# Optimization experiments

Measured on AMD Instinct MI355X. Metric: run time of the kernel, lower is better.

## Reference

```python
import jax, jax.numpy as jnp
import numpy as np

N, D, T, ET, E = 100000, 128, 3, 4, 250000


def gru_cell(m, h, w_ih, w_hh, b_ih, b_hh):
    # torch.nn.GRUCell semantics
    gi = m @ w_ih.T + b_ih          # [N, 3D]
    gh = h @ w_hh.T + b_hh          # [N, 3D]
    i_r, i_z, i_n = jnp.split(gi, 3, axis=1)
    h_r, h_z, h_n = jnp.split(gh, 3, axis=1)
    r = jax.nn.sigmoid(i_r + h_r)
    z = jax.nn.sigmoid(i_z + h_z)
    n = jnp.tanh(i_n + r * h_n)
    return (1.0 - z) * n + z * h


def setup_inputs() -> dict:
    key = jax.random.key(0)
    ks = jax.random.split(key, 10)
    x = jax.random.normal(ks[0], (N, D), dtype=jnp.float32)
    edge_row = jax.random.randint(ks[1], (ET, E), 0, N, dtype=jnp.int32)
    edge_col = jax.random.randint(ks[2], (ET, E), 0, N, dtype=jnp.int32)
    edge_val = jnp.ones((ET, E), dtype=jnp.float32)
    xav = float(np.sqrt(6.0 / (D + D)))  # xavier_uniform per (D,D) slice
    weight = jax.random.uniform(ks[3], (T, ET, D, D), jnp.float32, -xav, xav)
    bias_w = jax.random.uniform(ks[4], (T, ET, D), jnp.float32, -0.01, 0.01)
    s = float(1.0 / np.sqrt(D))  # GRUCell default init range
    w_ih = jax.random.uniform(ks[5], (3 * D, D), jnp.float32, -s, s)
    w_hh = jax.random.uniform(ks[6], (3 * D, D), jnp.float32, -s, s)
    b_ih = jax.random.uniform(ks[7], (3 * D,), jnp.float32, -s, s)
    b_hh = jax.random.uniform(ks[8], (3 * D,), jnp.float32, -s, s)
    return {"x": x, "edge_row": edge_row, "edge_col": edge_col,
            "edge_val": edge_val, "weight": weight, "bias_w": bias_w,
            "w_ih": w_ih, "w_hh": w_hh, "b_ih": b_ih, "b_hh": b_hh}


def reference(x, edge_row, edge_col, edge_val, weight, bias_w, w_ih, w_hh, b_ih, b_hh):
    n_nodes = x.shape[0]
    h = x  # input_dim == out_channels, no zero-padding needed
    num_t = weight.shape[0]

    def agg_one(m_e, col_e, row_e, val_e):
        # sparse.mm: out[row] += val * m[col]
        msg = m_e[col_e] * val_e[:, None]                 # [E, D]
        return jax.ops.segment_sum(msg, row_e, num_segments=n_nodes)

    for t in range(num_t):
        # per-edge-type dense transform: [ET, N, D]
        m = jnp.einsum('nd,edf->enf', h, weight[t]) + bias_w[t][:, None, :]
        agg = jax.vmap(agg_one)(m, edge_col, edge_row, edge_val)  # [ET, N, D]
        m_sum = agg.sum(axis=0)                                    # [N, D]
        h = gru_cell(m_sum, h, w_ih, w_hh, b_ih, b_hh)
    return h
```

## Files before the change

### kernel.cpp

```cpp
#include <hip/hip_runtime.h>
#include <stdint.h>

#define NN  100000
#define DD  128
#define TT  3
#define ETT 4
#define EE  250000
#define NCH 49
#define GRUGRID 512

typedef float  f32x4  __attribute__((ext_vector_type(4)));
typedef __bf16 bf16x8 __attribute__((ext_vector_type(8)));

__device__ __forceinline__ float bf2f(uint32_t u){ u <<= 16; return __builtin_bit_cast(float, u); }
__device__ __forceinline__ uint32_t f2bf(float f){
  uint32_t u = __builtin_bit_cast(uint32_t, f);
  return (u + 0x7FFFu + ((u >> 16) & 1u)) >> 16;
}
__device__ __forceinline__ f32x4 mfma16(bf16x8 a, bf16x8 b, f32x4 c){
  return __builtin_amdgcn_mfma_f32_16x16x32_bf16(a, b, c, 0, 0, 0);
}

__global__ void k_count(const int* __restrict__ erow, const float* __restrict__ eval,
                        int* __restrict__ counts, float* __restrict__ degval){
  int idx = blockIdx.x * 256 + threadIdx.x;
  if (idx >= ETT * EE) return;
  int e = idx / EE;
  int row = erow[idx];
  atomicAdd(&counts[e * NN + row], 1);
  atomicAdd(&degval[e * NN + row], eval[idx]);
}

__global__ void k_blksum(const int* __restrict__ counts, int* __restrict__ bsum){
  const int b = blockIdx.x, e = b / NCH, c = b % NCH;
  const int* p = counts + e * NN + c * 2048;
  int lim = NN - c * 2048; if (lim > 2048) lim = 2048;
  const int t = threadIdx.x;
  int s = 0;
  #pragma unroll
  for (int i = 0; i < 8; ++i){
    int idx = i * 256 + t;
    if (idx < lim) s += p[idx];
  }
  #pragma unroll
  for (int d = 32; d; d >>= 1) s += __shfl_down(s, d);
  __shared__ int wsum[4];
  if ((t & 63) == 0) wsum[t >> 6] = s;
  __syncthreads();
  if (t == 0) bsum[b] = wsum[0] + wsum[1] + wsum[2] + wsum[3];
}

__global__ void k_scanp(const int* __restrict__ bsum, int* __restrict__ bexc,
                        int* __restrict__ offsets){
  const int t = threadIdx.x, wid = t >> 6, l = t & 63;
  int v = (l < NCH) ? bsum[wid * NCH + l] : 0;
  int x = v;
  #pragma unroll
  for (int d = 1; d < 64; d <<= 1){ int y = __shfl_up(x, d); if (l >= d) x += y; }
  if (l < NCH) bexc[wid * NCH + l] = x - v;
  if (l == NCH - 1) offsets[wid * (NN + 1) + NN] = x;
}

__global__ void k_apply(const int* __restrict__ counts, const int* __restrict__ bexc,
                        int* __restrict__ offsets){
  const int b = blockIdx.x, e = b / NCH, c = b % NCH;
  const int* p = counts + e * NN + c * 2048;
  int* off = offsets + e * (NN + 1) + c * 2048;
  int lim = NN - c * 2048; if (lim > 2048) lim = 2048;
  const int t = threadIdx.x, l = t & 63, wid = t >> 6;
  __shared__ int wt[4];
  int v[8], s = 0;
  #pragma unroll
  for (int i = 0; i < 8; ++i){
    int idx = t * 8 + i;
    v[i] = (idx < lim) ? p[idx] : 0; s += v[i];
  }
  int x = s;
  #pragma unroll
  for (int d = 1; d < 64; d <<= 1){ int y = __shfl_up(x, d); if (l >= d) x += y; }
  if (l == 63) wt[wid] = x;
  __syncthreads();
  int wexc = 0;
  #pragma unroll
  for (int k = 0; k < 4; ++k) if (k < wid) wexc += wt[k];
  int te = bexc[b] + wexc + (x - s);
  #pragma unroll
  for (int i = 0; i < 8; ++i){
    int idx = t * 8 + i;
    if (idx < lim) off[idx] = te;
    te += v[i];
  }
}

__global__ void k_fill(const int* __restrict__ erow, const int* __restrict__ ecol,
                       const float* __restrict__ eval, const int* __restrict__ offsets,
                       int* __restrict__ cursor, uint2* __restrict__ sedge){
  int idx = blockIdx.x * 256 + threadIdx.x;
  if (idx >= ETT * EE) return;
  int e = idx / EE;
  int row = erow[idx];
  int pos = atomicAdd(&cursor[e * NN + row], 1);
  int o = offsets[e * (NN + 1) + row] + pos;
  sedge[e * EE + o] = make_uint2((uint32_t)ecol[idx], __builtin_bit_cast(uint32_t, eval[idx]));
}

__global__ void k_conv_x(const float* __restrict__ x, uint16_t* __restrict__ hbf){
  int idx = blockIdx.x * 256 + threadIdx.x;
  const float4* xp = (const float4*)x;
  float4 a = xp[idx * 2], b = xp[idx * 2 + 1];
  uint32_t p0 = f2bf(a.x) | (f2bf(a.y) << 16);
  uint32_t p1 = f2bf(a.z) | (f2bf(a.w) << 16);
  uint32_t p2 = f2bf(b.x) | (f2bf(b.y) << 16);
  uint32_t p3 = f2bf(b.z) | (f2bf(b.w) << 16);
  ((uint4*)hbf)[idx] = make_uint4(p0, p1, p2, p3);
}

__global__ void k_conv_w(const float* __restrict__ weight, const float* __restrict__ wih,
                         const float* __restrict__ whh, const float* __restrict__ bih,
                         const float* __restrict__ bhh, uint16_t* __restrict__ wcatT,
                         uint16_t* __restrict__ wihb, uint16_t* __restrict__ whhb,
                         float* __restrict__ bcomb){
  int idx = blockIdx.x * 256 + threadIdx.x;
  if (idx < TT * 128 * 512){
    int t = idx / 65536; int rem = idx - t * 65536;
    int f = rem >> 9; int u = rem & 511;
    int e = u >> 7; int d = u & 127;
    wcatT[idx] = (uint16_t)f2bf(weight[(((t * 4 + e) * 128 + d) << 7) + f]);
  }
  if (idx < 384 * 128){
    wihb[idx] = (uint16_t)f2bf(wih[idx]);
    whhb[idx] = (uint16_t)f2bf(whh[idx]);
  }
  if (idx < 256) bcomb[idx] = bih[idx] + bhh[idx];
}

#define ACC8(val, u) \
  acc[0] += val * bf2f(u.x & 0xffffu); acc[1] += val * bf2f(u.x >> 16); \
  acc[2] += val * bf2f(u.y & 0xffffu); acc[3] += val * bf2f(u.y >> 16); \
  acc[4] += val * bf2f(u.z & 0xffffu); acc[5] += val * bf2f(u.z >> 16); \
  acc[6] += val * bf2f(u.w & 0xffffu); acc[7] += val * bf2f(u.w >> 16);

__global__ __launch_bounds__(256, 8) void k_agg_gemm(
    const uint16_t* __restrict__ hbf, const int* __restrict__ offsets,
    const uint2* __restrict__ sedge, const float* __restrict__ degval,
    const float* __restrict__ bias_w, const uint16_t* __restrict__ wcatT_t,
    int tstep, uint16_t* __restrict__ m_out)
{
  __shared__ uint16_t aggT[16 * 512];
  const int tid = threadIdx.x;
  const int node0 = blockIdx.x * 16;

  {
    const int nl = tid >> 4, q = tid & 15;
    const int n = node0 + nl;
    #pragma unroll 1
    for (int e = 0; e < ETT; ++e){
      float acc[8];
      #pragma unroll
      for (int i = 0; i < 8; ++i) acc[i] = 0.f;
      const int s  = offsets[e * (NN + 1) + n];
      const int en = offsets[e * (NN + 1) + n + 1];
      const uint2* ep = sedge + (size_t)e * EE;
      #pragma unroll 1
      for (int i = s; i < en; i += 4){
        const int last = en - 1;
        const int i1 = (i + 1 < last) ? i + 1 : last;
        const int i2 = (i + 2 < last) ? i + 2 : last;
        const int i3 = (i + 3 < last) ? i + 3 : last;
        const uint2 cv0 = ep[i], cv1 = ep[i1], cv2 = ep[i2], cv3 = ep[i3];
        const float v0 = __builtin_bit_cast(float, cv0.y);
        const float v1 = (i + 1 <= last) ? __builtin_bit_cast(float, cv1.y) : 0.f;
        const float v2 = (i + 2 <= last) ? __builtin_bit_cast(float, cv2.y) : 0.f;
        const float v3 = (i + 3 <= last) ? __builtin_bit_cast(float, cv3.y) : 0.f;
        const uint4 u0 = *(const uint4*)(hbf + (size_t)cv0.x * DD + q * 8);
        const uint4 u1 = *(const uint4*)(hbf + (size_t)cv1.x * DD + q * 8);
        const uint4 u2 = *(const uint4*)(hbf + (size_t)cv2.x * DD + q * 8);
        const uint4 u3 = *(const uint4*)(hbf + (size_t)cv3.x * DD + q * 8);
        ACC8(v0, u0); ACC8(v1, u1); ACC8(v2, u2); ACC8(v3, u3);
      }
      const int c  = e * 16 + q;
      const int cs = c ^ (nl & 7);
      uint32_t p0 = f2bf(acc[0]) | (f2bf(acc[1]) << 16);
      uint32_t p1 = f2bf(acc[2]) | (f2bf(acc[3]) << 16);
      uint32_t p2 = f2bf(acc[4]) | (f2bf(acc[5]) << 16);
      uint32_t p3 = f2bf(acc[6]) | (f2bf(acc[7]) << 16);
      *(uint4*)&aggT[nl * 512 + cs * 8] = make_uint4(p0, p1, p2, p3);
    }
  }
  __syncthreads();

  const int lane = tid & 63, w = tid >> 6;
  const int rlo = lane & 15, kg = lane >> 4;
  f32x4 C[2];
  C[0] = f32x4{0.f, 0.f, 0.f, 0.f};
  C[1] = f32x4{0.f, 0.f, 0.f, 0.f};

  #pragma unroll
  for (int ks = 0; ks < 16; ++ks){
    const int cs = (ks * 4 + kg) ^ (rlo & 7);
    bf16x8 a = __builtin_bit_cast(bf16x8, *(const uint4*)&aggT[rlo * 512 + cs * 8]);
    #pragma unroll
    for (int ft = 0; ft < 2; ++ft){
      const int f = w * 32 + ft * 16 + rlo;
      bf16x8 b = __builtin_bit_cast(bf16x8, *(const uint4*)(wcatT_t + (size_t)f * 512 + ks * 32 + kg * 8));
      C[ft] = mfma16(a, b, C[ft]);
    }
  }

  const float* bwt = bias_w + tstep * (ETT * DD);
  float dv[4][4];
  #pragma unroll
  for (int r = 0; r < 4; ++r){
    const int n2 = node0 + kg * 4 + r;
    #pragma unroll
    for (int e = 0; e < 4; ++e) dv[e][r] = degval[e * NN + n2];
  }
  #pragma unroll
  for (int ft = 0; ft < 2; ++ft){
    const int f = w * 32 + ft * 16 + rlo;
    const float b0 = bwt[f], b1 = bwt[128 + f], b2 = bwt[256 + f], b3 = bwt[384 + f];
    #pragma unroll
    for (int r = 0; r < 4; ++r){
      const int n2 = node0 + kg * 4 + r;
      const float bias = dv[0][r]*b0 + dv[1][r]*b1 + dv[2][r]*b2 + dv[3][r]*b3;
      m_out[(size_t)n2 * DD + f] = (uint16_t)f2bf(C[ft][r] + bias);
    }
  }
}

__global__ __launch_bounds__(512, 2) void k_gru(
    const uint16_t* __restrict__ m_sum, const uint16_t* __restrict__ hsrc,
    uint16_t* __restrict__ hdst, const float* __restrict__ h_old,
    float* __restrict__ h_new, const uint16_t* __restrict__ wihb,
    const uint16_t* __restrict__ whhb, const float* __restrict__ bcomb,
    const float* __restrict__ b_ih, const float* __restrict__ b_hh)
{
  __shared__ uint4 mt[2][512];
  __shared__ uint4 ht[2][512];
  const int tid = threadIdx.x;
  const int lane = tid & 63, w = tid >> 6;
  const int rlo = lane & 15, kg = lane >> 4;

  bf16x8 wa[3][4], wb[3][4];
  #pragma unroll
  for (int g = 0; g < 3; ++g){
    const int j = g * 128 + w * 16 + rlo;
    #pragma unroll
    for (int ks = 0; ks < 4; ++ks){
      wa[g][ks] = __builtin_bit_cast(bf16x8, *(const uint4*)(wihb + j * 128 + ks * 32 + kg * 8));
      wb[g][ks] = __builtin_bit_cast(bf16x8, *(const uint4*)(whhb + j * 128 + ks * 32 + kg * 8));
    }
  }
  const int d0 = w * 16 + kg * 4;
  const f32x4 brz = *(const f32x4*)(bcomb + d0);
  const f32x4 bzz = *(const f32x4*)(bcomb + 128 + d0);
  const f32x4 bin = *(const f32x4*)(b_ih + 256 + d0);
  const f32x4 bhn = *(const f32x4*)(b_hh + 256 + d0);

  const int sn  = tid >> 4;
  const int scs = tid & 15;
  const int sc  = scs ^ (sn & 7);

  const int NT = NN / 32;
  int tile = blockIdx.x;
  {
    const size_t base = ((size_t)(tile * 32 + sn)) * DD + sc * 8;
    mt[0][sn * 16 + scs] = *(const uint4*)(m_sum + base);
    ht[0][sn * 16 + scs] = *(const uint4*)(hsrc + base);
  }
  __syncthreads();

  int buf = 0;
  #pragma unroll 1
  for (; tile < NT; tile += GRUGRID){
    const int ntile = tile + GRUGRID;
    const bool have = ntile < NT;
    uint4 mv, hv;
    if (have){
      const size_t nbase = ((size_t)(ntile * 32 + sn)) * DD + sc * 8;
      mv = *(const uint4*)(m_sum + nbase);
      hv = *(const uint4*)(hsrc + nbase);
    }

    f32x4 acc[3][2][2];
    #pragma unroll
    for (int g = 0; g < 3; ++g)
      #pragma unroll
      for (int m = 0; m < 2; ++m)
        #pragma unroll
        for (int ns = 0; ns < 2; ++ns) acc[g][m][ns] = f32x4{0.f,0.f,0.f,0.f};

    #pragma unroll
    for (int ks = 0; ks < 4; ++ks){
      #pragma unroll
      for (int ns = 0; ns < 2; ++ns){
        const int node = ns * 16 + rlo;
        const int cs = (ks * 4 + kg) ^ (node & 7);
        const bf16x8 bm = __builtin_bit_cast(bf16x8, mt[buf][node * 16 + cs]);
        const bf16x8 bh = __builtin_bit_cast(bf16x8, ht[buf][node * 16 + cs]);
        #pragma unroll
        for (int g = 0; g < 3; ++g){
          acc[g][0][ns] = mfma16(wa[g][ks], bm, acc[g][0][ns]);
          acc[g][1][ns] = mfma16(wb[g][ks], bh, acc[g][1][ns]);
        }
      }
    }

    #pragma unroll
    for (int ns = 0; ns < 2; ++ns){
      const int node = tile * 32 + ns * 16 + rlo;
      const f32x4 ho = *(const f32x4*)(h_old + (size_t)node * DD + d0);
      float hvv[4];
      #pragma unroll
      for (int r = 0; r < 4; ++r){
        const float rg = 1.f / (1.f + __expf(-(acc[0][0][ns][r] + acc[0][1][ns][r] + brz[r])));
        const float zg = 1.f / (1.f + __expf(-(acc[1][0][ns][r] + acc[1][1][ns][r] + bzz[r])));
        const float xa = (acc[2][0][ns][r] + bin[r]) + rg * (acc[2][1][ns][r] + bhn[r]);
        const float ng = 1.f - 2.f / (__expf(2.f * xa) + 1.f);
        hvv[r] = (1.f - zg) * ng + zg * ho[r];
      }
      *(f32x4*)(h_new + (size_t)node * DD + d0) = f32x4{hvv[0], hvv[1], hvv[2], hvv[3]};
      uint32_t p0 = f2bf(hvv[0]) | (f2bf(hvv[1]) << 16);
      uint32_t p1 = f2bf(hvv[2]) | (f2bf(hvv[3]) << 16);
      *(uint2*)(hdst + (size_t)node * DD + d0) = make_uint2(p0, p1);
    }

    if (have){
      mt[buf ^ 1][sn * 16 + scs] = mv;
      ht[buf ^ 1][sn * 16 + scs] = hv;
    }
    __syncthreads();
    buf ^= 1;
  }
}

extern "C" void kernel_launch(void* const* d_in, const int* in_sizes, int n_in,
                              void* d_out, int out_size, void* d_ws, size_t ws_size,
                              hipStream_t stream) {
  const float* x      = (const float*)d_in[0];
  const int*   erow   = (const int*)d_in[1];
  const int*   ecol   = (const int*)d_in[2];
  const float* eval   = (const float*)d_in[3];
  const float* weight = (const float*)d_in[4];
  const float* bias_w = (const float*)d_in[5];
  const float* wih    = (const float*)d_in[6];
  const float* whh    = (const float*)d_in[7];
  const float* bih    = (const float*)d_in[8];
  const float* bhh    = (const float*)d_in[9];
  float* out = (float*)d_out;
  char* ws = (char*)d_ws;

  size_t o = 0;
  auto alloc = [&](size_t bytes)->char*{ char* p = ws + o; o += (bytes + 255) & ~(size_t)255; return p; };
  int*      counts  = (int*)     alloc((size_t)ETT * NN * 4);
  int*      cursor  = (int*)     alloc((size_t)ETT * NN * 4);
  float*    degval  = (float*)   alloc((size_t)ETT * NN * 4);
  int*      offsets = (int*)     alloc((size_t)ETT * (NN + 1) * 4);
  int*      bsum    = (int*)     alloc((size_t)ETT * NCH * 4);
  int*      bexc    = (int*)     alloc((size_t)ETT * NCH * 4);
  uint2*    sedge   = (uint2*)   alloc((size_t)ETT * EE * 8);
  float*    hf      = (float*)   alloc((size_t)NN * DD * 4);
  uint16_t* hbf0    = (uint16_t*)alloc((size_t)NN * DD * 2);
  uint16_t* hbf1    = (uint16_t*)alloc((size_t)NN * DD * 2);
  uint16_t* msum    = (uint16_t*)alloc((size_t)NN * DD * 2);
  uint16_t* wcatT   = (uint16_t*)alloc((size_t)TT * 128 * 512 * 2);
  uint16_t* wihb    = (uint16_t*)alloc((size_t)384 * 128 * 2);
  uint16_t* whhb    = (uint16_t*)alloc((size_t)384 * 128 * 2);
  float*    bcomb   = (float*)   alloc((size_t)256 * 4);
  (void)ws_size; (void)in_sizes; (void)n_in; (void)out_size;

  hipMemsetAsync(counts, 0, (size_t)3 * ETT * NN * 4, stream);

  k_count<<<(ETT * EE + 255) / 256, 256, 0, stream>>>(erow, eval, counts, degval);
  k_blksum<<<ETT * NCH, 256, 0, stream>>>(counts, bsum);
  k_scanp<<<1, 256, 0, stream>>>(bsum, bexc, offsets);
  k_apply<<<ETT * NCH, 256, 0, stream>>>(counts, bexc, offsets);
  k_fill<<<(ETT * EE + 255) / 256, 256, 0, stream>>>(erow, ecol, eval, offsets, cursor, sedge);
  k_conv_x<<<(NN * DD / 8) / 256, 256, 0, stream>>>(x, hbf0);
  k_conv_w<<<(TT * 128 * 512 + 255) / 256, 256, 0, stream>>>(weight, wih, whh, bih, bhh,
                                                             wcatT, wihb, whhb, bcomb);

  uint16_t* hsrc = hbf0;
  uint16_t* hdst = hbf1;
  for (int t = 0; t < TT; ++t){
    k_agg_gemm<<<NN / 16, 256, 0, stream>>>(hsrc, offsets, sedge, degval,
                                            bias_w, wcatT + (size_t)t * 65536, t, msum);
    const float* hold = (t == 0) ? x : hf;
    float* hnew = (t == TT - 1) ? out : hf;
    k_gru<<<GRUGRID, 512, 0, stream>>>(msum, hsrc, hdst, hold, hnew,
                                       wihb, whhb, bcomb, bih, bhh);
    uint16_t* tmp = hsrc; hsrc = hdst; hdst = tmp;
  }
}
```

Before: 753.8 us.

## Merge per-edge-type CSRs into one CSR with type-tagged columns

Builds a single CSR over all edge types, packing the edge type into the high bits of the column index, so each node walks one edge list instead of four. The aggregation kernel now uses 32 threads per node reading 4 bf16 each, routes each contribution into one of four per-type accumulators by select, and processes 32 nodes per 1024-thread block, with each wave computing one 16x16 MFMA tile. This is meant to cut per-type loop overhead and offset loads and give more independent gathers in flight. In exchange it does 4x the FMAs per gathered value, and the larger blocks may reduce occupancy.

```diff
diff --git a/kernel.cpp b/kernel.cpp
--- a/kernel.cpp
+++ b/kernel.cpp
@@ -21,20 +21,20 @@
   return __builtin_amdgcn_mfma_f32_16x16x32_bf16(a, b, c, 0, 0, 0);
 }
 
-__global__ void k_count(const int* __restrict__ erow, const float* __restrict__ eval,
-                        int* __restrict__ counts, float* __restrict__ degval){
+__global__ void k_count_m(const int* __restrict__ erow, const float* __restrict__ eval,
+                          int* __restrict__ counts_m, float* __restrict__ degval){
   int idx = blockIdx.x * 256 + threadIdx.x;
   if (idx >= ETT * EE) return;
   int e = idx / EE;
   int row = erow[idx];
-  atomicAdd(&counts[e * NN + row], 1);
+  atomicAdd(&counts_m[row], 1);
   atomicAdd(&degval[e * NN + row], eval[idx]);
 }
 
-__global__ void k_blksum(const int* __restrict__ counts, int* __restrict__ bsum){
-  const int b = blockIdx.x, e = b / NCH, c = b % NCH;
-  const int* p = counts + e * NN + c * 2048;
-  int lim = NN - c * 2048; if (lim > 2048) lim = 2048;
+__global__ void k_blksum_m(const int* __restrict__ counts, int* __restrict__ bsum){
+  const int b = blockIdx.x;
+  const int* p = counts + b * 2048;
+  int lim = NN - b * 2048; if (lim > 2048) lim = 2048;
   const int t = threadIdx.x;
   int s = 0;
   #pragma unroll
@@ -50,23 +50,23 @@
   if (t == 0) bsum[b] = wsum[0] + wsum[1] + wsum[2] + wsum[3];
 }
 
-__global__ void k_scanp(const int* __restrict__ bsum, int* __restrict__ bexc,
-                        int* __restrict__ offsets){
-  const int t = threadIdx.x, wid = t >> 6, l = t & 63;
-  int v = (l < NCH) ? bsum[wid * NCH + l] : 0;
+__global__ void k_scanp_m(const int* __restrict__ bsum, int* __restrict__ bexc,
+                          int* __restrict__ offm){
+  const int l = threadIdx.x;
+  int v = (l < NCH) ? bsum[l] : 0;
   int x = v;
   #pragma unroll
   for (int d = 1; d < 64; d <<= 1){ int y = __shfl_up(x, d); if (l >= d) x += y; }
-  if (l < NCH) bexc[wid * NCH + l] = x - v;
-  if (l == NCH - 1) offsets[wid * (NN + 1) + NN] = x;
-}
-
-__global__ void k_apply(const int* __restrict__ counts, const int* __restrict__ bexc,
-                        int* __restrict__ offsets){
-  const int b = blockIdx.x, e = b / NCH, c = b % NCH;
-  const int* p = counts + e * NN + c * 2048;
-  int* off = offsets + e * (NN + 1) + c * 2048;
-  int lim = NN - c * 2048; if (lim > 2048) lim = 2048;
+  if (l < NCH) bexc[l] = x - v;
+  if (l == NCH - 1) offm[NN] = x;
+}
+
+__global__ void k_apply_m(const int* __restrict__ counts, const int* __restrict__ bexc,
+                          int* __restrict__ offm){
+  const int b = blockIdx.x;
+  const int* p = counts + b * 2048;
+  int* off = offm + b * 2048;
+  int lim = NN - b * 2048; if (lim > 2048) lim = 2048;
   const int t = threadIdx.x, l = t & 63, wid = t >> 6;
   __shared__ int wt[4];
   int v[8], s = 0;
@@ -92,16 +92,17 @@
   }
 }
 
-__global__ void k_fill(const int* __restrict__ erow, const int* __restrict__ ecol,
-                       const float* __restrict__ eval, const int* __restrict__ offsets,
-                       int* __restrict__ cursor, uint2* __restrict__ sedge){
+__global__ void k_fill_m(const int* __restrict__ erow, const int* __restrict__ ecol,
+                         const float* __restrict__ eval, const int* __restrict__ offm,
+                         int* __restrict__ cursor, uint2* __restrict__ sedge_m){
   int idx = blockIdx.x * 256 + threadIdx.x;
   if (idx >= ETT * EE) return;
   int e = idx / EE;
   int row = erow[idx];
-  int pos = atomicAdd(&cursor[e * NN + row], 1);
-  int o = offsets[e * (NN + 1) + row] + pos;
-  sedge[e * EE + o] = make_uint2((uint32_t)ecol[idx], __builtin_bit_cast(uint32_t, eval[idx]));
+  int pos = atomicAdd(&cursor[row], 1);
+  int o = offm[row] + pos;
+  sedge_m[o] = make_uint2((uint32_t)ecol[idx] | ((uint32_t)e << 20),
+                          __builtin_bit_cast(uint32_t, eval[idx]));
 }
 
 __global__ void k_conv_x(const float* __restrict__ x, uint16_t* __restrict__ hbf){
@@ -134,97 +135,95 @@
   if (idx < 256) bcomb[idx] = bih[idx] + bhh[idx];
 }
 
-#define ACC8(val, u) \
-  acc[0] += val * bf2f(u.x & 0xffffu); acc[1] += val * bf2f(u.x >> 16); \
-  acc[2] += val * bf2f(u.y & 0xffffu); acc[3] += val * bf2f(u.y >> 16); \
-  acc[4] += val * bf2f(u.z & 0xffffu); acc[5] += val * bf2f(u.z >> 16); \
-  acc[6] += val * bf2f(u.w & 0xffffu); acc[7] += val * bf2f(u.w >> 16);
-
-__global__ __launch_bounds__(256, 8) void k_agg_gemm(
-    const uint16_t* __restrict__ hbf, const int* __restrict__ offsets,
-    const uint2* __restrict__ sedge, const float* __restrict__ degval,
+#define PROC(ev, hv, vk) { \
+  const float f0 = bf2f(hv.x & 0xffffu), f1 = bf2f(hv.x >> 16); \
+  const float f2 = bf2f(hv.y & 0xffffu), f3 = bf2f(hv.y >> 16); \
+  const int et = (int)(ev.x >> 20); \
+  const float vs0 = (et == 0) ? vk : 0.f; \
+  const float vs1 = (et == 1) ? vk : 0.f; \
+  const float vs2 = (et == 2) ? vk : 0.f; \
+  const float vs3 = (et == 3) ? vk : 0.f; \
+  acc[0][0] += vs0*f0; acc[0][1] += vs0*f1; acc[0][2] += vs0*f2; acc[0][3] += vs0*f3; \
+  acc[1][0] += vs1*f0; acc[1][1] += vs1*f1; acc[1][2] += vs1*f2; acc[1][3] += vs1*f3; \
+  acc[2][0] += vs2*f0; acc[2][1] += vs2*f1; acc[2][2] += vs2*f2; acc[2][3] += vs2*f3; \
+  acc[3][0] += vs3*f0; acc[3][1] += vs3*f1; acc[3][2] += vs3*f2; acc[3][3] += vs3*f3; \
+}
+
+__global__ __launch_bounds__(1024, 8) void k_agg_gemm(
+    const uint16_t* __restrict__ hbf, const int* __restrict__ offm,
+    const uint2* __restrict__ sedge_m, const float* __restrict__ degval,
     const float* __restrict__ bias_w, const uint16_t* __restrict__ wcatT_t,
     int tstep, uint16_t* __restrict__ m_out)
 {
-  __shared__ uint16_t aggT[16 * 512];
+  __shared__ uint16_t aggT[32 * 512];
   const int tid = threadIdx.x;
-  const int node0 = blockIdx.x * 16;
+  const int node0 = blockIdx.x * 32;
 
   {
-    const int nl = tid >> 4, q = tid & 15;
+    const int nl = tid >> 5, q = tid & 31;
     const int n = node0 + nl;
+    float acc[4][4];
+    #pragma unroll
+    for (int e = 0; e < 4; ++e)
+      #pragma unroll
+      for (int d = 0; d < 4; ++d) acc[e][d] = 0.f;
+
+    const int s  = offm[n];
+    const int en = offm[n + 1];
     #pragma unroll 1
+    for (int i = s; i < en; i += 4){
+      const int last = en - 1;
+      const int i1 = (i + 1 < last) ? i + 1 : last;
+      const int i2 = (i + 2 < last) ? i + 2 : last;
+      const int i3 = (i + 3 < last) ? i + 3 : last;
+      const uint2 e0 = sedge_m[i],  e1 = sedge_m[i1];
+      const uint2 e2 = sedge_m[i2], e3 = sedge_m[i3];
+      const float v0 = __builtin_bit_cast(float, e0.y);
+      const float v1 = (i + 1 <= last) ? __builtin_bit_cast(float, e1.y) : 0.f;
+      const float v2 = (i + 2 <= last) ? __builtin_bit_cast(float, e2.y) : 0.f;
+      const float v3 = (i + 3 <= last) ? __builtin_bit_cast(float, e3.y) : 0.f;
+      const uint2 h0 = *(const uint2*)(hbf + (size_t)(e0.x & 0xFFFFFu) * DD + q * 4);
+      const uint2 h1 = *(const uint2*)(hbf + (size_t)(e1.x & 0xFFFFFu) * DD + q * 4);
+      const uint2 h2 = *(const uint2*)(hbf + (size_t)(e2.x & 0xFFFFFu) * DD + q * 4);
+      const uint2 h3 = *(const uint2*)(hbf + (size_t)(e3.x & 0xFFFFFu) * DD + q * 4);
+      PROC(e0, h0, v0); PROC(e1, h1, v1); PROC(e2, h2, v2); PROC(e3, h3, v3);
+    }
+
+    #pragma unroll
     for (int e = 0; e < ETT; ++e){
-      float acc[8];
-      #pragma unroll
-      for (int i = 0; i < 8; ++i) acc[i] = 0.f;
-      const int s  = offsets[e * (NN + 1) + n];
-      const int en = offsets[e * (NN + 1) + n + 1];
-      const uint2* ep = sedge + (size_t)e * EE;
-      #pragma unroll 1
-      for (int i = s; i < en; i += 4){
-        const int last = en - 1;
-        const int i1 = (i + 1 < last) ? i + 1 : last;
-        const int i2 = (i + 2 < last) ? i + 2 : last;
-        const int i3 = (i + 3 < last) ? i + 3 : last;
-        const uint2 cv0 = ep[i], cv1 = ep[i1], cv2 = ep[i2], cv3 = ep[i3];
-        const float v0 = __builtin_bit_cast(float, cv0.y);
-        const float v1 = (i + 1 <= last) ? __builtin_bit_cast(float, cv1.y) : 0.f;
-        const float v2 = (i + 2 <= last) ? __builtin_bit_cast(float, cv2.y) : 0.f;
-        const float v3 = (i + 3 <= last) ? __builtin_bit_cast(float, cv3.y) : 0.f;
-        const uint4 u0 = *(const uint4*)(hbf + (size_t)cv0.x * DD + q * 8);
-        const uint4 u1 = *(const uint4*)(hbf + (size_t)cv1.x * DD + q * 8);
-        const uint4 u2 = *(const uint4*)(hbf + (size_t)cv2.x * DD + q * 8);
-        const uint4 u3 = *(const uint4*)(hbf + (size_t)cv3.x * DD + q * 8);
-        ACC8(v0, u0); ACC8(v1, u1); ACC8(v2, u2); ACC8(v3, u3);
-      }
-      const int c  = e * 16 + q;
+      const int c  = e * 16 + (q >> 1);
       const int cs = c ^ (nl & 7);
-      uint32_t p0 = f2bf(acc[0]) | (f2bf(acc[1]) << 16);
-      uint32_t p1 = f2bf(acc[2]) | (f2bf(acc[3]) << 16);
-      uint32_t p2 = f2bf(acc[4]) | (f2bf(acc[5]) << 16);
-      uint32_t p3 = f2bf(acc[6]) | (f2bf(acc[7]) << 16);
-      *(uint4*)&aggT[nl * 512 + cs * 8] = make_uint4(p0, p1, p2, p3);
+      uint32_t p0 = f2bf(acc[e][0]) | (f2bf(acc[e][1]) << 16);
+      uint32_t p1 = f2bf(acc[e][2]) | (f2bf(acc[e][3]) << 16);
+      *(uint2*)&aggT[nl * 512 + cs * 8 + (q & 1) * 4] = make_uint2(p0, p1);
     }
   }
   __syncthreads();
 
   const int lane = tid & 63, w = tid >> 6;
   const int rlo = lane & 15, kg = lane >> 4;
-  f32x4 C[2];
-  C[0] = f32x4{0.f, 0.f, 0.f, 0.f};
-  C[1] = f32x4{0.f, 0.f, 0.f, 0.f};
+  const int rt = w & 1, fc = w >> 1;
+  const int rowA = rt * 16 + rlo;
+  f32x4 C = f32x4{0.f, 0.f, 0.f, 0.f};
 
   #pragma unroll
   for (int ks = 0; ks < 16; ++ks){
-    const int cs = (ks * 4 + kg) ^ (rlo & 7);
-    bf16x8 a = __builtin_bit_cast(bf16x8, *(const uint4*)&aggT[rlo * 512 + cs * 8]);
-    #pragma unroll
-    for (int ft = 0; ft < 2; ++ft){
-      const int f = w * 32 + ft * 16 + rlo;
-      bf16x8 b = __builtin_bit_cast(bf16x8, *(const uint4*)(wcatT_t + (size_t)f * 512 + ks * 32 + kg * 8));
-      C[ft] = mfma16(a, b, C[ft]);
-    }
+    const int cs = (ks * 4 + kg) ^ (rowA & 7);
+    bf16x8 a = __builtin_bit_cast(bf16x8, *(const uint4*)&aggT[rowA * 512 + cs * 8]);
+    bf16x8 b = __builtin_bit_cast(bf16x8,
+        *(const uint4*)(wcatT_t + (size_t)(fc * 16 + rlo) * 512 + ks * 32 + kg * 8));
+    C = mfma16(a, b, C);
   }
 
   const float* bwt = bias_w + tstep * (ETT * DD);
-  float dv[4][4];
+  const int f = fc * 16 + rlo;
+  const float b0 = bwt[f], b1 = bwt[128 + f], b2 = bwt[256 + f], b3 = bwt[384 + f];
   #pragma unroll
   for (int r = 0; r < 4; ++r){
-    const int n2 = node0 + kg * 4 + r;
-    #pragma unroll
-    for (int e = 0; e < 4; ++e) dv[e][r] = degval[e * NN + n2];
-  }
-  #pragma unroll
-  for (int ft = 0; ft < 2; ++ft){
-    const int f = w * 32 + ft * 16 + rlo;
-    const float b0 = bwt[f], b1 = bwt[128 + f], b2 = bwt[256 + f], b3 = bwt[384 + f];
-    #pragma unroll
-    for (int r = 0; r < 4; ++r){
-      const int n2 = node0 + kg * 4 + r;
-      const float bias = dv[0][r]*b0 + dv[1][r]*b1 + dv[2][r]*b2 + dv[3][r]*b3;
-      m_out[(size_t)n2 * DD + f] = (uint16_t)f2bf(C[ft][r] + bias);
-    }
+    const int n2 = node0 + rt * 16 + kg * 4 + r;
+    const float bias = degval[n2] * b0 + degval[NN + n2] * b1
+                     + degval[2 * NN + n2] * b2 + degval[3 * NN + n2] * b3;
+    m_out[(size_t)n2 * DD + f] = (uint16_t)f2bf(C[r] + bias);
   }
 }
 
@@ -352,30 +351,31 @@
 
   size_t o = 0;
   auto alloc = [&](size_t bytes)->char*{ char* p = ws + o; o += (bytes + 255) & ~(size_t)255; return p; };
-  int*      counts  = (int*)     alloc((size_t)ETT * NN * 4);
-  int*      cursor  = (int*)     alloc((size_t)ETT * NN * 4);
-  float*    degval  = (float*)   alloc((size_t)ETT * NN * 4);
-  int*      offsets = (int*)     alloc((size_t)ETT * (NN + 1) * 4);
-  int*      bsum    = (int*)     alloc((size_t)ETT * NCH * 4);
-  int*      bexc    = (int*)     alloc((size_t)ETT * NCH * 4);
-  uint2*    sedge   = (uint2*)   alloc((size_t)ETT * EE * 8);
-  float*    hf      = (float*)   alloc((size_t)NN * DD * 4);
-  uint16_t* hbf0    = (uint16_t*)alloc((size_t)NN * DD * 2);
-  uint16_t* hbf1    = (uint16_t*)alloc((size_t)NN * DD * 2);
-  uint16_t* msum    = (uint16_t*)alloc((size_t)NN * DD * 2);
-  uint16_t* wcatT   = (uint16_t*)alloc((size_t)TT * 128 * 512 * 2);
-  uint16_t* wihb    = (uint16_t*)alloc((size_t)384 * 128 * 2);
-  uint16_t* whhb    = (uint16_t*)alloc((size_t)384 * 128 * 2);
-  float*    bcomb   = (float*)   alloc((size_t)256 * 4);
+  int*      counts_m = (int*)     alloc((size_t)NN * 4);
+  int*      cursor_m = (int*)     alloc((size_t)NN * 4);
+  float*    degval   = (float*)   alloc((size_t)ETT * NN * 4);
+  int*      offm     = (int*)     alloc((size_t)(NN + 1) * 4);
+  int*      bsum     = (int*)     alloc((size_t)NCH * 4);
+  int*      bexc     = (int*)     alloc((size_t)NCH * 4);
+  uint2*    sedge_m  = (uint2*)   alloc((size_t)ETT * EE * 8);
+  float*    hf       = (float*)   alloc((size_t)NN * DD * 4);
+  uint16_t* hbf0     = (uint16_t*)alloc((size_t)NN * DD * 2);
+  uint16_t* hbf1     = (uint16_t*)alloc((size_t)NN * DD * 2);
+  uint16_t* msum     = (uint16_t*)alloc((size_t)NN * DD * 2);
+  uint16_t* wcatT    = (uint16_t*)alloc((size_t)TT * 128 * 512 * 2);
+  uint16_t* wihb     = (uint16_t*)alloc((size_t)384 * 128 * 2);
+  uint16_t* whhb     = (uint16_t*)alloc((size_t)384 * 128 * 2);
+  float*    bcomb    = (float*)   alloc((size_t)256 * 4);
   (void)ws_size; (void)in_sizes; (void)n_in; (void)out_size;
 
-  hipMemsetAsync(counts, 0, (size_t)3 * ETT * NN * 4, stream);
-
-  k_count<<<(ETT * EE + 255) / 256, 256, 0, stream>>>(erow, eval, counts, degval);
-  k_blksum<<<ETT * NCH, 256, 0, stream>>>(counts, bsum);
-  k_scanp<<<1, 256, 0, stream>>>(bsum, bexc, offsets);
-  k_apply<<<ETT * NCH, 256, 0, stream>>>(counts, bexc, offsets);
-  k_fill<<<(ETT * EE + 255) / 256, 256, 0, stream>>>(erow, ecol, eval, offsets, cursor, sedge);
+  const size_t zspan = (size_t)((char*)degval - (char*)counts_m) + (size_t)ETT * NN * 4;
+  hipMemsetAsync(counts_m, 0, zspan, stream);
+
+  k_count_m<<<(ETT * EE + 255) / 256, 256, 0, stream>>>(erow, eval, counts_m, degval);
+  k_blksum_m<<<NCH, 256, 0, stream>>>(counts_m, bsum);
+  k_scanp_m<<<1, 64, 0, stream>>>(bsum, bexc, offm);
+  k_apply_m<<<NCH, 256, 0, stream>>>(counts_m, bexc, offm);
+  k_fill_m<<<(ETT * EE + 255) / 256, 256, 0, stream>>>(erow, ecol, eval, offm, cursor_m, sedge_m);
   k_conv_x<<<(NN * DD / 8) / 256, 256, 0, stream>>>(x, hbf0);
   k_conv_w<<<(TT * 128 * 512 + 255) / 256, 256, 0, stream>>>(weight, wih, whh, bih, bhh,
                                                              wcatT, wihb, whhb, bcomb);
@@ -383,8 +383,8 @@
   uint16_t* hsrc = hbf0;
   uint16_t* hdst = hbf1;
   for (int t = 0; t < TT; ++t){
-    k_agg_gemm<<<NN / 16, 256, 0, stream>>>(hsrc, offsets, sedge, degval,
-                                            bias_w, wcatT + (size_t)t * 65536, t, msum);
+    k_agg_gemm<<<NN / 32, 1024, 0, stream>>>(hsrc, offm, sedge_m, degval,
+                                             bias_w, wcatT + (size_t)t * 65536, t, msum);
     const float* hold = (t == 0) ? x : hf;
     float* hnew = (t == TT - 1) ? out : hf;
     k_gru<<<GRUGRID, 512, 0, stream>>>(msum, hsrc, hdst, hold, hnew,
```

New measurement: 780.3 us. 3.5% more time.
